# Performance work log

Hardware: AMD Instinct MI355X
Metric: run time of the kernel (lower is better)

Reference implementation:

```python
import jax, jax.numpy as jnp
import numpy as np

KS = 3      # kernel_size
PAD = 1     # padding
DIL = 2     # dilation


def conv2d(x, w, b=None, stride=1, padding=0):
    out = jax.lax.conv_general_dilated(
        x, w, (stride, stride), [(padding, padding)] * 2,
        dimension_numbers=("NCHW", "OIHW", "NCHW"))
    if b is not None:
        out = out + b[None, :, None, None]
    return out


def setup_inputs() -> dict:
    key = jax.random.key(0)
    ks = jax.random.split(key, 6)
    b, inc, outc, H, W = 2, 256, 256, 96, 96
    x = jax.random.normal(ks[0], (b, inc, H, W), jnp.float32)
    w_p = jax.random.normal(ks[1], (2 * KS * KS, inc, 3, 3), jnp.float32) * 0.01
    b_p = jax.random.normal(ks[2], (2 * KS * KS,), jnp.float32) * 0.01
    w_ad = jax.random.normal(ks[3], (KS, inc, 3, 3), jnp.float32) * 0.01
    b_ad = jax.random.normal(ks[4], (KS,), jnp.float32) * 0.01
    w_conv = jax.random.normal(ks[5], (outc, inc, KS, KS), jnp.float32) * 0.02
    return {"x": x, "w_p": w_p, "b_p": b_p, "w_ad": w_ad, "b_ad": b_ad, "w_conv": w_conv}


def reference(x, w_p, b_p, w_ad, b_ad, w_conv):
    b, c, H, W = x.shape
    N = KS * KS

    offset = conv2d(x, w_p, b_p, stride=1, padding=1)                    # [b,2N,H,W]
    ad_base = 1.0 - jax.nn.sigmoid(conv2d(x, w_ad, b_ad, stride=1, padding=1))  # [b,KS,H,W]
    ad = jnp.tile(ad_base, (1, 2 * KS, 1, 1)) * DIL                      # [b,2N,H,W]

    # p_n: per-kernel-tap offsets (x-part first, then y-part), meshgrid 'ij'
    r = jnp.arange(-(KS - 1) // 2, (KS - 1) // 2 + 1, dtype=jnp.float32)
    pnx, pny = jnp.meshgrid(r, r, indexing="ij")
    p_n = jnp.concatenate([pnx.ravel(), pny.ravel()])[None, :, None, None]  # [1,2N,1,1]

    # p_0: base sampling grid in padded-image coords (starts at 1)
    p0x = jnp.broadcast_to(jnp.arange(1, H + 1, dtype=jnp.float32)[:, None], (H, W))
    p0y = jnp.broadcast_to(jnp.arange(1, W + 1, dtype=jnp.float32)[None, :], (H, W))
    p_0 = jnp.concatenate([jnp.tile(p0x[None, None], (1, N, 1, 1)),
                           jnp.tile(p0y[None, None], (1, N, 1, 1))], axis=1)  # [1,2N,H,W]

    p = p_0 + p_n + offset + ad * p_n                                    # [b,2N,H,W]
    p = jnp.transpose(p, (0, 2, 3, 1))                                   # [b,H,W,2N]

    xp = jnp.pad(x, ((0, 0), (0, 0), (PAD, PAD), (PAD, PAD)))
    Hp, Wp = xp.shape[2], xp.shape[3]

    q_lt = jnp.floor(jax.lax.stop_gradient(p))
    q_rb = q_lt + 1

    def clampxy(q):
        return jnp.concatenate([jnp.clip(q[..., :N], 0, Hp - 1),
                                jnp.clip(q[..., N:], 0, Wp - 1)], -1).astype(jnp.int32)

    q_lt = clampxy(q_lt)
    q_rb = clampxy(q_rb)
    q_lb = jnp.concatenate([q_lt[..., :N], q_rb[..., N:]], -1)
    q_rt = jnp.concatenate([q_rb[..., :N], q_lt[..., N:]], -1)

    mask = jnp.concatenate(
        [(p[..., :N] < PAD) | (p[..., :N] > Hp - 1 - PAD),
         (p[..., N:] < PAD) | (p[..., N:] > Wp - 1 - PAD)], -1)
    mask = jax.lax.stop_gradient(mask).astype(p.dtype)
    floor_p = p - (p - jnp.floor(p))  # == floor(p) but with zero gradient, as in torch
    p = p * (1 - mask) + floor_p * mask
    p = jnp.concatenate([jnp.clip(p[..., :N], 0, Hp - 1),
                         jnp.clip(p[..., N:], 0, Wp - 1)], -1)

    px, py = p[..., :N], p[..., N:]
    f = lambda q: q.astype(p.dtype)
    g_lt = (1 + (f(q_lt[..., :N]) - px)) * (1 + (f(q_lt[..., N:]) - py))
    g_rb = (1 - (f(q_rb[..., :N]) - px)) * (1 - (f(q_rb[..., N:]) - py))
    g_lb = (1 + (f(q_lb[..., :N]) - px)) * (1 - (f(q_lb[..., N:]) - py))
    g_rt = (1 - (f(q_rt[..., :N]) - px)) * (1 + (f(q_rt[..., N:]) - py))

    xf = xp.reshape(b, c, Hp * Wp)

    def gather(xb, q):  # xb [c,L], q [H,W,2N] -> [c,H,W,N]
        idx = q[..., :N] * Wp + q[..., N:]
        return xb[:, idx]

    gq = jax.vmap(gather)
    x_lt = gq(xf, q_lt)
    x_rb = gq(xf, q_rb)
    x_lb = gq(xf, q_lb)
    x_rt = gq(xf, q_rt)

    x_off = (g_lt[:, None] * x_lt + g_rb[:, None] * x_rb +
             g_lb[:, None] * x_lb + g_rt[:, None] * x_rt)  # [b,c,H,W,N]

    # N index k = kx*KS + ky -> place at (i*KS+kx, j*KS+ky)
    x_off = x_off.reshape(b, c, H, W, KS, KS)
    x_off = jnp.transpose(x_off, (0, 1, 2, 4, 3, 5)).reshape(b, c, H * KS, W * KS)

    return conv2d(x_off, w_conv, None, stride=KS, padding=0)  # [b,outc,H,W]
```

## Files before the change

kernel.cpp:

```cpp
#include <hip/hip_runtime.h>
#include <math.h>

typedef unsigned short u16;
typedef unsigned int   u32;

typedef __attribute__((ext_vector_type(8))) _Float16 f16x8;
typedef __attribute__((ext_vector_type(4))) float    f32x4;

#define NB   2
#define C    256
#define H    96
#define W    96
#define HW   (H*W)
#define HP   98
#define OC   256
#define KDIM (9*C)
#define NS   (NB*HW)

#define XP_OFF    0
#define AHI_OFF   19668992
#define ALO_OFF   20848640
#define A2HI_OFF  22028288
#define A2LO_OFF  22175744
#define OFF2_OFF  22323200
#define IDX_OFF   23871488
#define G_OFF     26525696

__device__ __forceinline__ u16 h2u(_Float16 h) {
  return __builtin_bit_cast(unsigned short, h);
}
__device__ __forceinline__ void split16(float v, u16& hi, u16& lo) {
  _Float16 h = (_Float16)v;
  float r = v - (float)h;
  _Float16 l = (_Float16)r;
  hi = h2u(h); lo = h2u(l);
}
__device__ __forceinline__ void sync_lds() {
  asm volatile("s_waitcnt lgkmcnt(0)\n\ts_barrier" ::: "memory");
}

__global__ __launch_bounds__(256) void prep1(
    const float* __restrict__ x, const float* __restrict__ w_p,
    const float* __restrict__ w_ad, const float* __restrict__ w_conv,
    float* __restrict__ xp,
    u16* __restrict__ A_hi, u16* __restrict__ A_lo,
    u16* __restrict__ A2_hi, u16* __restrict__ A2_lo) {
  __shared__ float smem[64*65];
  int bx = blockIdx.x;
  int tid = threadIdx.x;

  if (bx < 1152) {
    int pb = bx;
    int n = pb / 576; int r = pb % 576;
    int cb = r / 144; int hwb = r % 144;
    int c0 = cb * 64, hw0 = hwb * 64;
    int ii = tid & 63; int cl4 = tid >> 6;
    #pragma unroll
    for (int r2 = 0; r2 < 16; r2++) {
      int c_l = cl4*16 + r2;
      smem[c_l*65 + ii] = x[(size_t)(n*C + c0 + c_l)*HW + hw0 + ii];
    }
    __syncthreads();
    int hw = hw0 + ii;
    int h = hw / W, w = hw % W;
    float* dst = xp + ((size_t)(n*HP + h + 1)*HP + (w + 1))*C + c0 + cl4*16;
    #pragma unroll
    for (int q = 0; q < 4; q++) {
      *(float4*)(dst + q*4) = make_float4(smem[(cl4*16 + q*4 + 0)*65 + ii],
                                          smem[(cl4*16 + q*4 + 1)*65 + ii],
                                          smem[(cl4*16 + q*4 + 2)*65 + ii],
                                          smem[(cl4*16 + q*4 + 3)*65 + ii]);
    }

  } else if (bx < 1440) {
    int pb = bx - 1152;
    int t = pb*256 + tid;
    int e0 = t*8;
    int lane = (e0 >> 3) & 63;
    int mi   = (e0 >> 9) & 3;
    int mw   = (e0 >> 11) & 1;
    int rr   = e0 >> 12; int itg = rr % 72; int mo = rr / 72;
    int o = mo*128 + mw*64 + mi*16 + (lane & 15);
    int kcb = itg*32 + (lane >> 4)*8;
    #pragma unroll
    for (int j2 = 0; j2 < 8; j2++) {
      int kc = kcb + j2; int k = kc >> 8; int c = kc & 255;
      float a = w_conv[((size_t)o*C + c)*9 + k];
      u16 hi, lo; split16(a, hi, lo);
      A_hi[e0 + j2] = hi; A_lo[e0 + j2] = lo;
    }

  } else {
    int pb = bx - 1440;
    int t = pb*256 + tid;
    int e0 = t*8;
    int lane = (e0 >> 3) & 63;
    int mi   = (e0 >> 9) & 1;
    int itg  = e0 >> 10;
    int o = mi*16 + (lane & 15);
    int kcb = itg*32 + (lane >> 4)*8;
    #pragma unroll
    for (int j2 = 0; j2 < 8; j2++) {
      int kc = kcb + j2; int tap = kc >> 8; int c = kc & 255;
      float a = 0.f;
      if (o < 18)       a = w_p [((size_t)o*C + c)*9 + tap];
      else if (o < 21)  a = w_ad[((size_t)(o-18)*C + c)*9 + tap];
      u16 hi, lo; split16(a, hi, lo);
      A2_hi[e0 + j2] = hi; A2_lo[e0 + j2] = lo;
    }
  }
}

__global__ __launch_bounds__(256) void conv_mfma(
    const u16* __restrict__ A2_hi, const u16* __restrict__ A2_lo,
    const float* __restrict__ xp, float* __restrict__ off2) {
  __shared__ u16 Bh[2][64*40];
  __shared__ u16 Bl[2][64*40];
  int bx = blockIdx.x;
  int xcd = bx & 7; int jj = bx >> 3;
  int kh = jj & 1; int sbl = jj >> 1;
  int sb = xcd*36 + sbl;
  int s0 = sb * 64;
  int tid = threadIdx.x;
  int wave = tid >> 6, lane = tid & 63;
  int l16 = lane & 15, quad = lane >> 4;

  f32x4 acc[2];
  f32x4 z4 = {0.f, 0.f, 0.f, 0.f};
  acc[0] = z4; acc[1] = z4;

  int s_l = tid >> 2; int cs = (tid & 3) * 8;
  int sg = s0 + s_l;
  int n = sg / HW; int hw = sg % HW;
  int h = hw / W, w = hw % W;
  const float* sbase = xp + ((size_t)(n*HP + h)*HP + w)*C;

  for (int it = 0; it < 36; it++) {
    int itg = kh*36 + it;
    int tap = itg >> 3;
    int di = tap / 3, dj = tap % 3;
    int c0k = (itg & 7) * 32;
    uint4 aH[2], aL[2];
    #pragma unroll
    for (int mi = 0; mi < 2; mi++) {
      size_t off = ((size_t)(itg*2 + mi) << 9) + lane*8;
      aH[mi] = *(const uint4*)(A2_hi + off);
      aL[mi] = *(const uint4*)(A2_lo + off);
    }
    const float* p0 = sbase + (di*HP + dj)*C + c0k + cs;
    float4 ta = *(const float4*)(p0), tb = *(const float4*)(p0 + 4);
    float v[8] = {ta.x, ta.y, ta.z, ta.w, tb.x, tb.y, tb.z, tb.w};
    u16 hb[8], lb[8];
    #pragma unroll
    for (int j = 0; j < 8; j++) split16(v[j], hb[j], lb[j]);
    uint4 bph, bpl;
    bph.x = (u32)hb[0] | ((u32)hb[1] << 16); bph.y = (u32)hb[2] | ((u32)hb[3] << 16);
    bph.z = (u32)hb[4] | ((u32)hb[5] << 16); bph.w = (u32)hb[6] | ((u32)hb[7] << 16);
    bpl.x = (u32)lb[0] | ((u32)lb[1] << 16); bpl.y = (u32)lb[2] | ((u32)lb[3] << 16);
    bpl.z = (u32)lb[4] | ((u32)lb[5] << 16); bpl.w = (u32)lb[6] | ((u32)lb[7] << 16);
    int buf = it & 1;
    *(uint4*)(&Bh[buf][s_l*40 + cs]) = bph;
    *(uint4*)(&Bl[buf][s_l*40 + cs]) = bpl;
    sync_lds();
    int rr = (wave*16 + l16)*40 + quad*8;
    f16x8 bfh = *(const f16x8*)(&Bh[buf][rr]);
    f16x8 bfl = *(const f16x8*)(&Bl[buf][rr]);
    #pragma unroll
    for (int mi = 0; mi < 2; mi++) {
      f16x8 fh = __builtin_bit_cast(f16x8, aH[mi]);
      f16x8 fl = __builtin_bit_cast(f16x8, aL[mi]);
      acc[mi] = __builtin_amdgcn_mfma_f32_16x16x32_f16(fh, bfh, acc[mi], 0, 0, 0);
      acc[mi] = __builtin_amdgcn_mfma_f32_16x16x32_f16(fh, bfl, acc[mi], 0, 0, 0);
      acc[mi] = __builtin_amdgcn_mfma_f32_16x16x32_f16(fl, bfh, acc[mi], 0, 0, 0);
    }
  }
  int sout = s0 + wave*16 + l16;
  #pragma unroll
  for (int mi = 0; mi < 2; mi++)
    #pragma unroll
    for (int rr2 = 0; rr2 < 4; rr2++) {
      int o = mi*16 + quad*4 + rr2;
      if (o < 21)
        atomicAdd(&off2[(size_t)o*NS + sout], acc[mi][rr2]);
    }
}

__global__ __launch_bounds__(256) void taps2(
    const float* __restrict__ off2, const float* __restrict__ b_p,
    const float* __restrict__ b_ad,
    int* __restrict__ idx_arr, float* __restrict__ g_arr) {
  int e = blockIdx.x * 256 + threadIdx.x;
  int k = e / NS; int s = e % NS;
  int n = s / HW; int hw = s % HW;
  int h = hw / W, w = hw % W;
  float offx = off2[(size_t)k*NS + s]            + b_p[k];
  float offy = off2[(size_t)(k+9)*NS + s]        + b_p[k+9];
  float za   = off2[(size_t)(18 + (k%3))*NS + s] + b_ad[k % 3];
  float a2 = 2.0f / (1.0f + expf(za));

  float ri = (float)(k / 3) - 1.0f, rj = (float)(k % 3) - 1.0f;
  float px = (float)(h + 1) + ri + offx + a2 * ri;
  float py = (float)(w + 1) + rj + offy + a2 * rj;
  float fx = floorf(px), fy = floorf(py);
  int qltx = min(max((int)fx, 0), 97);
  int qlty = min(max((int)fy, 0), 97);
  int qrbx = min(max((int)fx + 1, 0), 97);
  int qrby = min(max((int)fy + 1, 0), 97);
  bool mx = (px < 1.0f) || (px > 96.0f);
  bool my = (py < 1.0f) || (py > 96.0f);
  float pxm = mx ? fx : px;
  float pym = my ? fy : py;
  pxm = fminf(fmaxf(pxm, 0.f), 97.f);
  pym = fminf(fmaxf(pym, 0.f), 97.f);
  float glx = 1.0f + ((float)qltx - pxm);
  float grx = 1.0f - ((float)qrbx - pxm);
  float gly = 1.0f + ((float)qlty - pym);
  float gry = 1.0f - ((float)qrby - pym);
  int base = n * HP * HP * C;
  int4 qi;
  qi.x = base + (qltx*HP + qlty)*C;
  qi.y = base + (qrbx*HP + qrby)*C;
  qi.z = base + (qltx*HP + qrby)*C;
  qi.w = base + (qrbx*HP + qlty)*C;
  float4 gg = make_float4(glx*gly, grx*gry, glx*gry, grx*gly);
  *(int4*)(idx_arr + (size_t)e*4) = qi;
  *(float4*)(g_arr  + (size_t)e*4) = gg;
}

__global__ __launch_bounds__(256) void gemm_def(
    const u16* __restrict__ A_hi, const u16* __restrict__ A_lo,
    const float* __restrict__ xp,
    const int* __restrict__ idx_arr, const float* __restrict__ g_arr,
    float* __restrict__ out) {
  __shared__ u16 Bh[2][64*40];
  __shared__ u16 Bl[2][64*40];
  int bx = blockIdx.x;
  int xcd = bx & 7; int jj = bx >> 3;
  int kh = jj & 1; int sbl = jj >> 1;
  int sb = xcd*36 + sbl;
  int s0 = sb * 64;
  int n = s0 / HW; int hw0 = s0 % HW;
  int tid = threadIdx.x;
  int wave = tid >> 6, lane = tid & 63;
  int l16 = lane & 15, quad = lane >> 4;
  int mo = wave >> 1, mw = wave & 1;

  f32x4 acc[4][4];
  f32x4 z4 = {0.f, 0.f, 0.f, 0.f};
  #pragma unroll
  for (int i = 0; i < 4; i++)
    { acc[i][0] = z4; acc[i][1] = z4; acc[i][2] = z4; acc[i][3] = z4; }

  int s_l = tid >> 2; int cs = (tid & 3) * 8;
  int sg = s0 + s_l;

  int4 qi; float4 gg;
  for (int it = 0; it < 36; it++) {
    int itg = kh*36 + it;
    int c0k = (itg & 7) * 32;
    if (it == 0 || (itg & 7) == 0) {
      int k = itg >> 3;
      qi = *(const int4*)(idx_arr + ((size_t)k*NS + sg)*4);
      gg = *(const float4*)(g_arr  + ((size_t)k*NS + sg)*4);
    }
    uint4 aH[4], aL[4];
    int abase = ((mo*72 + itg)*2 + mw)*4;
    #pragma unroll
    for (int mi = 0; mi < 4; mi++) {
      size_t off = ((size_t)(abase + mi) << 9) + lane*8;
      aH[mi] = *(const uint4*)(A_hi + off);
      aL[mi] = *(const uint4*)(A_lo + off);
    }
    const float* p0 = xp + qi.x + c0k + cs;
    const float* p1 = xp + qi.y + c0k + cs;
    const float* p2 = xp + qi.z + c0k + cs;
    const float* p3 = xp + qi.w + c0k + cs;
    float4 t0a = *(const float4*)(p0), t0b = *(const float4*)(p0 + 4);
    float4 t1a = *(const float4*)(p1), t1b = *(const float4*)(p1 + 4);
    float4 t2a = *(const float4*)(p2), t2b = *(const float4*)(p2 + 4);
    float4 t3a = *(const float4*)(p3), t3b = *(const float4*)(p3 + 4);
    float v[8];
    v[0] = gg.x*t0a.x + gg.y*t1a.x + gg.z*t2a.x + gg.w*t3a.x;
    v[1] = gg.x*t0a.y + gg.y*t1a.y + gg.z*t2a.y + gg.w*t3a.y;
    v[2] = gg.x*t0a.z + gg.y*t1a.z + gg.z*t2a.z + gg.w*t3a.z;
    v[3] = gg.x*t0a.w + gg.y*t1a.w + gg.z*t2a.w + gg.w*t3a.w;
    v[4] = gg.x*t0b.x + gg.y*t1b.x + gg.z*t2b.x + gg.w*t3b.x;
    v[5] = gg.x*t0b.y + gg.y*t1b.y + gg.z*t2b.y + gg.w*t3b.y;
    v[6] = gg.x*t0b.z + gg.y*t1b.z + gg.z*t2b.z + gg.w*t3b.z;
    v[7] = gg.x*t0b.w + gg.y*t1b.w + gg.z*t2b.w + gg.w*t3b.w;
    u16 hb[8], lb[8];
    #pragma unroll
    for (int j = 0; j < 8; j++) split16(v[j], hb[j], lb[j]);
    uint4 bph, bpl;
    bph.x = (u32)hb[0] | ((u32)hb[1] << 16); bph.y = (u32)hb[2] | ((u32)hb[3] << 16);
    bph.z = (u32)hb[4] | ((u32)hb[5] << 16); bph.w = (u32)hb[6] | ((u32)hb[7] << 16);
    bpl.x = (u32)lb[0] | ((u32)lb[1] << 16); bpl.y = (u32)lb[2] | ((u32)lb[3] << 16);
    bpl.z = (u32)lb[4] | ((u32)lb[5] << 16); bpl.w = (u32)lb[6] | ((u32)lb[7] << 16);
    int buf = it & 1;
    *(uint4*)(&Bh[buf][s_l*40 + cs]) = bph;
    *(uint4*)(&Bl[buf][s_l*40 + cs]) = bpl;
    sync_lds();
    f16x8 bfh[4], bfl[4];
    #pragma unroll
    for (int ni = 0; ni < 4; ni++) {
      int rr = (ni*16 + l16)*40 + quad*8;
      bfh[ni] = *(const f16x8*)(&Bh[buf][rr]);
      bfl[ni] = *(const f16x8*)(&Bl[buf][rr]);
    }
    #pragma unroll
    for (int mi = 0; mi < 4; mi++) {
      f16x8 fh = __builtin_bit_cast(f16x8, aH[mi]);
      f16x8 fl = __builtin_bit_cast(f16x8, aL[mi]);
      #pragma unroll
      for (int ni = 0; ni < 4; ni++) {
        acc[mi][ni] = __builtin_amdgcn_mfma_f32_16x16x32_f16(fh, bfh[ni], acc[mi][ni], 0, 0, 0);
        acc[mi][ni] = __builtin_amdgcn_mfma_f32_16x16x32_f16(fh, bfl[ni], acc[mi][ni], 0, 0, 0);
        acc[mi][ni] = __builtin_amdgcn_mfma_f32_16x16x32_f16(fl, bfh[ni], acc[mi][ni], 0, 0, 0);
      }
    }
  }
  #pragma unroll
  for (int mi = 0; mi < 4; mi++)
    #pragma unroll
    for (int ni = 0; ni < 4; ni++) {
      int hw = hw0 + ni*16 + l16;
      #pragma unroll
      for (int rr = 0; rr < 4; rr++) {
        int o = wave*64 + mi*16 + quad*4 + rr;
        atomicAdd(&out[(size_t)(n*OC + o)*HW + hw], acc[mi][ni][rr]);
      }
    }
}

extern "C" void kernel_launch(void* const* d_in, const int* in_sizes, int n_in,
                              void* d_out, int out_size, void* d_ws, size_t ws_size,
                              hipStream_t stream) {
  const float* x      = (const float*)d_in[0];
  const float* w_p    = (const float*)d_in[1];
  const float* b_p    = (const float*)d_in[2];
  const float* w_ad   = (const float*)d_in[3];
  const float* b_ad   = (const float*)d_in[4];
  const float* w_conv = (const float*)d_in[5];
  float* out = (float*)d_out;

  char* ws = (char*)d_ws;
  float* xp      = (float*)(ws + XP_OFF);
  u16*   A_hi    = (u16*)  (ws + AHI_OFF);
  u16*   A_lo    = (u16*)  (ws + ALO_OFF);
  u16*   A2_hi   = (u16*)  (ws + A2HI_OFF);
  u16*   A2_lo   = (u16*)  (ws + A2LO_OFF);
  float* off2    = (float*)(ws + OFF2_OFF);
  int*   idx_arr = (int*)  (ws + IDX_OFF);
  float* g_arr   = (float*)(ws + G_OFF);

  hipMemsetAsync(xp, 0, (size_t)NB*HP*HP*C*sizeof(float), stream);
  hipMemsetAsync(off2, 0, (size_t)21*NS*sizeof(float), stream);
  hipMemsetAsync(out, 0, (size_t)out_size*sizeof(float), stream);

  prep1    <<<1476, 256, 0, stream>>>(x, w_p, w_ad, w_conv, xp, A_hi, A_lo, A2_hi, A2_lo);
  conv_mfma<<<576,  256, 0, stream>>>(A2_hi, A2_lo, xp, off2);
  taps2    <<<648,  256, 0, stream>>>(off2, b_p, b_ad, idx_arr, g_arr);
  gemm_def <<<576,  256, 0, stream>>>(A_hi, A_lo, xp, idx_arr, g_arr, out);
}
```

Measured before the change: 220.1 us.

## Software-pipeline global loads of weights and gathered inputs across K iterations

Both the offset-conv GEMM and the main deformable GEMM kernels now prefetch the next iteration's A fragments and input/gather values into registers, overlapping them with the current iteration's MFMA work. The LDS write is done from the prefetched registers at the top of each loop. This is meant to hide global-memory latency behind the tensor-core math. In exchange it raises register pressure (extra uint4 and float4 buffers), which could lower occupancy or cause spills.

Result: slower. 290.8 us (+32.1%).

```diff
diff --git a/kernel.cpp b/kernel.cpp
--- a/kernel.cpp
+++ b/kernel.cpp
@@ -38,6 +38,40 @@
 __device__ __forceinline__ void sync_lds() {
   asm volatile("s_waitcnt lgkmcnt(0)\n\ts_barrier" ::: "memory");
 }
+
+#define BW_GATHER(T, G, BUFI) do { \
+  float v0_ = (G).x*(T)[0].x + (G).y*(T)[2].x + (G).z*(T)[4].x + (G).w*(T)[6].x; \
+  float v1_ = (G).x*(T)[0].y + (G).y*(T)[2].y + (G).z*(T)[4].y + (G).w*(T)[6].y; \
+  float v2_ = (G).x*(T)[0].z + (G).y*(T)[2].z + (G).z*(T)[4].z + (G).w*(T)[6].z; \
+  float v3_ = (G).x*(T)[0].w + (G).y*(T)[2].w + (G).z*(T)[4].w + (G).w*(T)[6].w; \
+  float v4_ = (G).x*(T)[1].x + (G).y*(T)[3].x + (G).z*(T)[5].x + (G).w*(T)[7].x; \
+  float v5_ = (G).x*(T)[1].y + (G).y*(T)[3].y + (G).z*(T)[5].y + (G).w*(T)[7].y; \
+  float v6_ = (G).x*(T)[1].z + (G).y*(T)[3].z + (G).z*(T)[5].z + (G).w*(T)[7].z; \
+  float v7_ = (G).x*(T)[1].w + (G).y*(T)[3].w + (G).z*(T)[5].w + (G).w*(T)[7].w; \
+  u16 h0_,l0_,h1_,l1_,h2_,l2_,h3_,l3_,h4_,l4_,h5_,l5_,h6_,l6_,h7_,l7_; \
+  split16(v0_,h0_,l0_); split16(v1_,h1_,l1_); split16(v2_,h2_,l2_); split16(v3_,h3_,l3_); \
+  split16(v4_,h4_,l4_); split16(v5_,h5_,l5_); split16(v6_,h6_,l6_); split16(v7_,h7_,l7_); \
+  uint4 bph_, bpl_; \
+  bph_.x = (u32)h0_ | ((u32)h1_ << 16); bph_.y = (u32)h2_ | ((u32)h3_ << 16); \
+  bph_.z = (u32)h4_ | ((u32)h5_ << 16); bph_.w = (u32)h6_ | ((u32)h7_ << 16); \
+  bpl_.x = (u32)l0_ | ((u32)l1_ << 16); bpl_.y = (u32)l2_ | ((u32)l3_ << 16); \
+  bpl_.z = (u32)l4_ | ((u32)l5_ << 16); bpl_.w = (u32)l6_ | ((u32)l7_ << 16); \
+  *(uint4*)(&Bh[BUFI][s_l*40 + cs]) = bph_; \
+  *(uint4*)(&Bl[BUFI][s_l*40 + cs]) = bpl_; \
+} while (0)
+
+#define BW_RAW(TA, TB, BUFI) do { \
+  u16 h0_,l0_,h1_,l1_,h2_,l2_,h3_,l3_,h4_,l4_,h5_,l5_,h6_,l6_,h7_,l7_; \
+  split16((TA).x,h0_,l0_); split16((TA).y,h1_,l1_); split16((TA).z,h2_,l2_); split16((TA).w,h3_,l3_); \
+  split16((TB).x,h4_,l4_); split16((TB).y,h5_,l5_); split16((TB).z,h6_,l6_); split16((TB).w,h7_,l7_); \
+  uint4 bph_, bpl_; \
+  bph_.x = (u32)h0_ | ((u32)h1_ << 16); bph_.y = (u32)h2_ | ((u32)h3_ << 16); \
+  bph_.z = (u32)h4_ | ((u32)h5_ << 16); bph_.w = (u32)h6_ | ((u32)h7_ << 16); \
+  bpl_.x = (u32)l0_ | ((u32)l1_ << 16); bpl_.y = (u32)l2_ | ((u32)l3_ << 16); \
+  bpl_.z = (u32)l4_ | ((u32)l5_ << 16); bpl_.w = (u32)l6_ | ((u32)l7_ << 16); \
+  *(uint4*)(&Bh[BUFI][s_l*40 + cs]) = bph_; \
+  *(uint4*)(&Bl[BUFI][s_l*40 + cs]) = bpl_; \
+} while (0)
 
 __global__ __launch_bounds__(256) void prep1(
     const float* __restrict__ x, const float* __restrict__ w_p,
@@ -135,36 +169,45 @@
   int h = hw / W, w = hw % W;
   const float* sbase = xp + ((size_t)(n*HP + h)*HP + w)*C;
 
-  for (int it = 0; it < 36; it++) {
-    int itg = kh*36 + it;
-    int tap = itg >> 3;
-    int di = tap / 3, dj = tap % 3;
-    int c0k = (itg & 7) * 32;
-    uint4 aH[2], aL[2];
+  const int itbase = kh*36;
+  uint4 aH[2], aL[2];
+  float4 tca, tcb;
+  {
+    int itg = itbase;
     #pragma unroll
     for (int mi = 0; mi < 2; mi++) {
       size_t off = ((size_t)(itg*2 + mi) << 9) + lane*8;
       aH[mi] = *(const uint4*)(A2_hi + off);
       aL[mi] = *(const uint4*)(A2_lo + off);
     }
+    int tap = itg >> 3; int di = tap / 3, dj = tap % 3;
+    int c0k = (itg & 7) * 32;
     const float* p0 = sbase + (di*HP + dj)*C + c0k + cs;
-    float4 ta = *(const float4*)(p0), tb = *(const float4*)(p0 + 4);
-    float v[8] = {ta.x, ta.y, ta.z, ta.w, tb.x, tb.y, tb.z, tb.w};
-    u16 hb[8], lb[8];
-    #pragma unroll
-    for (int j = 0; j < 8; j++) split16(v[j], hb[j], lb[j]);
-    uint4 bph, bpl;
-    bph.x = (u32)hb[0] | ((u32)hb[1] << 16); bph.y = (u32)hb[2] | ((u32)hb[3] << 16);
-    bph.z = (u32)hb[4] | ((u32)hb[5] << 16); bph.w = (u32)hb[6] | ((u32)hb[7] << 16);
-    bpl.x = (u32)lb[0] | ((u32)lb[1] << 16); bpl.y = (u32)lb[2] | ((u32)lb[3] << 16);
-    bpl.z = (u32)lb[4] | ((u32)lb[5] << 16); bpl.w = (u32)lb[6] | ((u32)lb[7] << 16);
+    tca = *(const float4*)(p0); tcb = *(const float4*)(p0 + 4);
+  }
+
+  #pragma unroll 2
+  for (int it = 0; it < 36; it++) {
     int buf = it & 1;
-    *(uint4*)(&Bh[buf][s_l*40 + cs]) = bph;
-    *(uint4*)(&Bl[buf][s_l*40 + cs]) = bpl;
+    BW_RAW(tca, tcb, buf);
     sync_lds();
     int rr = (wave*16 + l16)*40 + quad*8;
     f16x8 bfh = *(const f16x8*)(&Bh[buf][rr]);
     f16x8 bfl = *(const f16x8*)(&Bl[buf][rr]);
+    uint4 aHn[2], aLn[2]; float4 tna, tnb;
+    if (it < 35) {
+      int itn = itbase + it + 1;
+      #pragma unroll
+      for (int mi = 0; mi < 2; mi++) {
+        size_t off = ((size_t)(itn*2 + mi) << 9) + lane*8;
+        aHn[mi] = *(const uint4*)(A2_hi + off);
+        aLn[mi] = *(const uint4*)(A2_lo + off);
+      }
+      int tap = itn >> 3; int di = tap / 3, dj = tap % 3;
+      int c0k = (itn & 7) * 32;
+      const float* p0 = sbase + (di*HP + dj)*C + c0k + cs;
+      tna = *(const float4*)(p0); tnb = *(const float4*)(p0 + 4);
+    }
     #pragma unroll
     for (int mi = 0; mi < 2; mi++) {
       f16x8 fh = __builtin_bit_cast(f16x8, aH[mi]);
@@ -172,6 +215,11 @@
       acc[mi] = __builtin_amdgcn_mfma_f32_16x16x32_f16(fh, bfh, acc[mi], 0, 0, 0);
       acc[mi] = __builtin_amdgcn_mfma_f32_16x16x32_f16(fh, bfl, acc[mi], 0, 0, 0);
       acc[mi] = __builtin_amdgcn_mfma_f32_16x16x32_f16(fl, bfh, acc[mi], 0, 0, 0);
+    }
+    if (it < 35) {
+      aH[0] = aHn[0]; aH[1] = aHn[1];
+      aL[0] = aLn[0]; aL[1] = aLn[1];
+      tca = tna; tcb = tnb;
     }
   }
   int sout = s0 + wave*16 + l16;
@@ -254,16 +302,16 @@
   int s_l = tid >> 2; int cs = (tid & 3) * 8;
   int sg = s0 + s_l;
 
+  const int itbase = kh*36;
   int4 qi; float4 gg;
-  for (int it = 0; it < 36; it++) {
-    int itg = kh*36 + it;
-    int c0k = (itg & 7) * 32;
-    if (it == 0 || (itg & 7) == 0) {
-      int k = itg >> 3;
-      qi = *(const int4*)(idx_arr + ((size_t)k*NS + sg)*4);
-      gg = *(const float4*)(g_arr  + ((size_t)k*NS + sg)*4);
-    }
-    uint4 aH[4], aL[4];
+  uint4 aH[4], aL[4];
+  float4 tc[8];
+
+  {
+    int itg = itbase;
+    int k = itg >> 3;
+    qi = *(const int4*)(idx_arr + ((size_t)k*NS + sg)*4);
+    gg = *(const float4*)(g_arr  + ((size_t)k*NS + sg)*4);
     int abase = ((mo*72 + itg)*2 + mw)*4;
     #pragma unroll
     for (int mi = 0; mi < 4; mi++) {
@@ -271,34 +319,21 @@
       aH[mi] = *(const uint4*)(A_hi + off);
       aL[mi] = *(const uint4*)(A_lo + off);
     }
+    int c0k = (itg & 7) * 32;
     const float* p0 = xp + qi.x + c0k + cs;
     const float* p1 = xp + qi.y + c0k + cs;
     const float* p2 = xp + qi.z + c0k + cs;
     const float* p3 = xp + qi.w + c0k + cs;
-    float4 t0a = *(const float4*)(p0), t0b = *(const float4*)(p0 + 4);
-    float4 t1a = *(const float4*)(p1), t1b = *(const float4*)(p1 + 4);
-    float4 t2a = *(const float4*)(p2), t2b = *(const float4*)(p2 + 4);
-    float4 t3a = *(const float4*)(p3), t3b = *(const float4*)(p3 + 4);
-    float v[8];
-    v[0] = gg.x*t0a.x + gg.y*t1a.x + gg.z*t2a.x + gg.w*t3a.x;
-    v[1] = gg.x*t0a.y + gg.y*t1a.y + gg.z*t2a.y + gg.w*t3a.y;
-    v[2] = gg.x*t0a.z + gg.y*t1a.z + gg.z*t2a.z + gg.w*t3a.z;
-    v[3] = gg.x*t0a.w + gg.y*t1a.w + gg.z*t2a.w + gg.w*t3a.w;
-    v[4] = gg.x*t0b.x + gg.y*t1b.x + gg.z*t2b.x + gg.w*t3b.x;
-    v[5] = gg.x*t0b.y + gg.y*t1b.y + gg.z*t2b.y + gg.w*t3b.y;
-    v[6] = gg.x*t0b.z + gg.y*t1b.z + gg.z*t2b.z + gg.w*t3b.z;
-    v[7] = gg.x*t0b.w + gg.y*t1b.w + gg.z*t2b.w + gg.w*t3b.w;
-    u16 hb[8], lb[8];
-    #pragma unroll
-    for (int j = 0; j < 8; j++) split16(v[j], hb[j], lb[j]);
-    uint4 bph, bpl;
-    bph.x = (u32)hb[0] | ((u32)hb[1] << 16); bph.y = (u32)hb[2] | ((u32)hb[3] << 16);
-    bph.z = (u32)hb[4] | ((u32)hb[5] << 16); bph.w = (u32)hb[6] | ((u32)hb[7] << 16);
-    bpl.x = (u32)lb[0] | ((u32)lb[1] << 16); bpl.y = (u32)lb[2] | ((u32)lb[3] << 16);
-    bpl.z = (u32)lb[4] | ((u32)lb[5] << 16); bpl.w = (u32)lb[6] | ((u32)lb[7] << 16);
+    tc[0] = *(const float4*)(p0); tc[1] = *(const float4*)(p0 + 4);
+    tc[2] = *(const float4*)(p1); tc[3] = *(const float4*)(p1 + 4);
+    tc[4] = *(const float4*)(p2); tc[5] = *(const float4*)(p2 + 4);
+    tc[6] = *(const float4*)(p3); tc[7] = *(const float4*)(p3 + 4);
+  }
+
+  #pragma unroll 2
+  for (int it = 0; it < 36; it++) {
     int buf = it & 1;
-    *(uint4*)(&Bh[buf][s_l*40 + cs]) = bph;
-    *(uint4*)(&Bl[buf][s_l*40 + cs]) = bpl;
+    BW_GATHER(tc, gg, buf);
     sync_lds();
     f16x8 bfh[4], bfl[4];
     #pragma unroll
@@ -306,6 +341,33 @@
       int rr = (ni*16 + l16)*40 + quad*8;
       bfh[ni] = *(const f16x8*)(&Bh[buf][rr]);
       bfl[ni] = *(const f16x8*)(&Bl[buf][rr]);
+    }
+    int4 qin = qi; float4 ggn = gg;
+    uint4 aHn[4], aLn[4];
+    float4 tn[8];
+    if (it < 35) {
+      int itn = itbase + it + 1;
+      if ((itn & 7) == 0) {
+        int k = itn >> 3;
+        qin = *(const int4*)(idx_arr + ((size_t)k*NS + sg)*4);
+        ggn = *(const float4*)(g_arr  + ((size_t)k*NS + sg)*4);
+      }
+      int abase = ((mo*72 + itn)*2 + mw)*4;
+      #pragma unroll
+      for (int mi = 0; mi < 4; mi++) {
+        size_t off = ((size_t)(abase + mi) << 9) + lane*8;
+        aHn[mi] = *(const uint4*)(A_hi + off);
+        aLn[mi] = *(const uint4*)(A_lo + off);
+      }
+      int c0k = (itn & 7) * 32;
+      const float* p0 = xp + qin.x + c0k + cs;
+      const float* p1 = xp + qin.y + c0k + cs;
+      const float* p2 = xp + qin.z + c0k + cs;
+      const float* p3 = xp + qin.w + c0k + cs;
+      tn[0] = *(const float4*)(p0); tn[1] = *(const float4*)(p0 + 4);
+      tn[2] = *(const float4*)(p1); tn[3] = *(const float4*)(p1 + 4);
+      tn[4] = *(const float4*)(p2); tn[5] = *(const float4*)(p2 + 4);
+      tn[6] = *(const float4*)(p3); tn[7] = *(const float4*)(p3 + 4);
     }
     #pragma unroll
     for (int mi = 0; mi < 4; mi++) {
@@ -317,6 +379,13 @@
         acc[mi][ni] = __builtin_amdgcn_mfma_f32_16x16x32_f16(fh, bfl[ni], acc[mi][ni], 0, 0, 0);
         acc[mi][ni] = __builtin_amdgcn_mfma_f32_16x16x32_f16(fl, bfh[ni], acc[mi][ni], 0, 0, 0);
       }
+    }
+    if (it < 35) {
+      qi = qin; gg = ggn;
+      #pragma unroll
+      for (int mi = 0; mi < 4; mi++) { aH[mi] = aHn[mi]; aL[mi] = aLn[mi]; }
+      #pragma unroll
+      for (int j = 0; j < 8; j++) tc[j] = tn[j];
     }
   }
   #pragma unroll
```
